# Kernel optimization log

Measured on AMD Instinct MI355X. Metric: run time of the kernel, lower is better.

Reference implementation:

```python
import jax, jax.numpy as jnp
import numpy as np

N_HEAD, D_MODEL, D_HEAD = 16, 1024, 64
SEQ, BATCH = 1024, 8
SCALE = 1.0 / (D_HEAD ** 0.5)
LN_EPS = 1e-5


def setup_inputs() -> dict:
    key = jax.random.key(0)
    ks = jax.random.split(key, 16)
    dk = N_HEAD * D_HEAD  # == D_MODEL
    init_qkv = 1.0 / np.sqrt(D_MODEL)
    init_out = 1.0 / np.sqrt(dk)
    u = lambda k, shp, lo, hi: jax.random.uniform(k, shp, jnp.float32, lo, hi)
    inp = {
        'dec_inp': jax.random.normal(ks[0], (SEQ, BATCH, D_MODEL), jnp.float32),
        'attn_mask': jnp.triu(jnp.ones((SEQ, SEQ), dtype=bool), k=1),  # causal
        'query_mean': u(ks[1], (dk, D_MODEL), -init_qkv, init_qkv),
        'key_mean': u(ks[2], (dk, D_MODEL), -init_qkv, init_qkv),
        'value_mean': u(ks[3], (dk, D_MODEL), -init_qkv, init_qkv),
        'query_std': u(ks[4], (dk, D_MODEL), 2 * np.log(init_qkv), np.log(init_qkv)),
        'key_std': u(ks[5], (dk, D_MODEL), 2 * np.log(init_qkv), np.log(init_qkv)),
        'value_std': u(ks[6], (dk, D_MODEL), 2 * np.log(init_qkv), np.log(init_qkv)),
        'output_mean': u(ks[7], (D_MODEL, dk), -init_out, init_out),
        'output_std': u(ks[8], (D_MODEL, dk), 2 * np.log(init_out), np.log(init_out)),
        'ln_gamma': jnp.ones((D_MODEL,), jnp.float32),
        'ln_beta': jnp.zeros((D_MODEL,), jnp.float32),
        # per-forward reparameterization noise (training mode)
        'eps_q': jax.random.normal(ks[9], (dk, D_MODEL), jnp.float32),
        'eps_k': jax.random.normal(ks[10], (dk, D_MODEL), jnp.float32),
        'eps_v': jax.random.normal(ks[11], (dk, D_MODEL), jnp.float32),
        'eps_o': jax.random.normal(ks[12], (D_MODEL, dk), jnp.float32),
    }
    return inp


def _forward(dec_inp, query_mean, key_mean, value_mean, query_std, key_std,
             value_std, output_mean, output_std, ln_gamma, ln_beta,
             eps_q, eps_k, eps_v, eps_o, attn_mask):
    S, B, _ = dec_inp.shape
    # Bayesian weight sampling: w = mean + eps * exp(std)
    qw = query_mean + eps_q * jnp.exp(query_std)
    kw = key_mean + eps_k * jnp.exp(key_std)
    vw = value_mean + eps_v * jnp.exp(value_std)
    # NOTE: original code (bug kept for faithfulness) builds the output weight
    # from value_mean + output_diff, not output_mean.
    ow = value_mean + eps_o * jnp.exp(output_std)

    head_q = (dec_inp @ qw.T).reshape(S, B, N_HEAD, D_HEAD)
    head_k = (dec_inp @ kw.T).reshape(S, B, N_HEAD, D_HEAD)
    head_v = (dec_inp @ vw.T).reshape(S, B, N_HEAD, D_HEAD)

    score = jnp.einsum('ibnd,jbnd->ijbn', head_q, head_k) * SCALE
    score = jnp.where(attn_mask[:, :, None, None], -jnp.inf, score)
    prob = jax.nn.softmax(score, axis=1)  # softmax over j (key) axis
    attn_vec = jnp.einsum('ijbn,jbnd->ibnd', prob, head_v).reshape(S, B, N_HEAD * D_HEAD)

    attn_out = attn_vec @ ow.T
    x = dec_inp + attn_out
    mu = jnp.mean(x, axis=-1, keepdims=True)
    var = jnp.var(x, axis=-1, keepdims=True)
    output = (x - mu) * jax.lax.rsqrt(var + LN_EPS) * ln_gamma + ln_beta

    theta_mean = jnp.concatenate([query_mean, key_mean, value_mean, output_mean.T], -1)
    theta_std = jnp.concatenate([query_std, key_std, value_std, output_std.T], -1)
    kl = jnp.mean(theta_mean ** 2 - theta_std * 2.0 + jnp.exp(theta_std * 2.0)) / 2.0
    return output, kl


def reference(dec_inp, attn_mask, query_mean, key_mean, value_mean, query_std,
              key_std, value_std, output_mean, output_std, ln_gamma, ln_beta,
              eps_q, eps_k, eps_v, eps_o):
    return _forward(dec_inp, query_mean, key_mean, value_mean, query_std,
                    key_std, value_std, output_mean, output_std, ln_gamma,
                    ln_beta, eps_q, eps_k, eps_v, eps_o, attn_mask)
```

## Files before the change

kernel.cpp:

```cpp
#include <hip/hip_runtime.h>

typedef _Float16 f16x8 __attribute__((ext_vector_type(8)));
typedef _Float16 f16x4 __attribute__((ext_vector_type(4)));
typedef float    f32x4 __attribute__((ext_vector_type(4)));

static __device__ __forceinline__ f32x4 mfma16(f16x8 a, f16x8 b, f32x4 c) {
    return __builtin_amdgcn_mfma_f32_16x16x32_f16(a, b, c, 0, 0, 0);
}

static __device__ __forceinline__ void gload_lds16(const _Float16* g, _Float16* lds) {
    __builtin_amdgcn_global_load_lds(
        (const __attribute__((address_space(1))) unsigned int*)g,
        (__attribute__((address_space(3))) unsigned int*)lds, 16, 0, 0);
}

__global__ __launch_bounds__(256) void k_prep(
    const float* __restrict__ qm, const float* __restrict__ km, const float* __restrict__ vm,
    const float* __restrict__ qs, const float* __restrict__ ks, const float* __restrict__ vs,
    const float* __restrict__ om, const float* __restrict__ os,
    const float* __restrict__ eq, const float* __restrict__ ek,
    const float* __restrict__ ev, const float* __restrict__ eo,
    _Float16* __restrict__ wq, _Float16* __restrict__ wk,
    _Float16* __restrict__ wv, _Float16* __restrict__ wo,
    float* __restrict__ part,
    const float* __restrict__ dec, _Float16* __restrict__ xh)
{
    if (blockIdx.x >= 1024) {
        int base = (blockIdx.x - 1024) * 4096;
        #pragma unroll
        for (int rp = 0; rp < 4; ++rp) {
            int i = base + rp * 1024 + threadIdx.x * 4;
            float4 v = *(const float4*)&dec[i];
            f16x4 hv;
            hv[0] = (_Float16)v.x; hv[1] = (_Float16)v.y;
            hv[2] = (_Float16)v.z; hv[3] = (_Float16)v.w;
            *(f16x4*)&xh[i] = hv;
        }
        return;
    }
    int i = (blockIdx.x * 256 + threadIdx.x) * 4;
    f32x4 aqm = *(const f32x4*)&qm[i], akm = *(const f32x4*)&km[i], avm = *(const f32x4*)&vm[i];
    f32x4 aqs = *(const f32x4*)&qs[i], aks = *(const f32x4*)&ks[i], avs = *(const f32x4*)&vs[i];
    f32x4 aom = *(const f32x4*)&om[i], aos = *(const f32x4*)&os[i];
    f32x4 veq = *(const f32x4*)&eq[i], vek = *(const f32x4*)&ek[i];
    f32x4 vev = *(const f32x4*)&ev[i], veo = *(const f32x4*)&eo[i];
    f16x4 hq, hk, hv, ho;
    float t = 0.f;
    #pragma unroll
    for (int j = 0; j < 4; ++j) {
        hq[j] = (_Float16)(aqm[j] + veq[j] * __expf(aqs[j]));
        hk[j] = (_Float16)(akm[j] + vek[j] * __expf(aks[j]));
        hv[j] = (_Float16)(avm[j] + vev[j] * __expf(avs[j]));
        ho[j] = (_Float16)(avm[j] + veo[j] * __expf(aos[j]));
        t += aqm[j]*aqm[j] - 2.f*aqs[j] + __expf(2.f*aqs[j])
           + akm[j]*akm[j] - 2.f*aks[j] + __expf(2.f*aks[j])
           + avm[j]*avm[j] - 2.f*avs[j] + __expf(2.f*avs[j])
           + aom[j]*aom[j] - 2.f*aos[j] + __expf(2.f*aos[j]);
    }
    *(f16x4*)&wq[i] = hq;
    *(f16x4*)&wk[i] = hk;
    *(f16x4*)&wv[i] = hv;
    *(f16x4*)&wo[i] = ho;
    #pragma unroll
    for (int m = 1; m < 64; m <<= 1) t += __shfl_xor(t, m, 64);
    __shared__ float red[4];
    int w = threadIdx.x >> 6, lane = threadIdx.x & 63;
    if (lane == 0) red[w] = t;
    __syncthreads();
    if (threadIdx.x == 0) part[blockIdx.x] = red[0] + red[1] + red[2] + red[3];
}

__global__ __launch_bounds__(256) void k_gemm(
    const _Float16* __restrict__ A, const _Float16* __restrict__ Bp,
    _Float16* __restrict__ Cp, const float* __restrict__ resid,
    float* __restrict__ xout, int mode, float sc)
{
    __shared__ __align__(16) _Float16 As[128 * 64];
    __shared__ __align__(16) _Float16 Bs[128 * 64];
    const int K = 1024, N = 1024;
    int flat = blockIdx.y * 8 + blockIdx.x;
    int xcd = flat & 7, j = flat >> 3;
    int tM = (xcd * 8 + (j & 7)) * 128;
    int tN = (j >> 3) * 128;
    int tid = threadIdx.x, w = tid >> 6, lane = tid & 63;
    int wm = w & 1, wn = w >> 1;
    int q = lane >> 4, r = lane & 15;
    int csrc = ((lane & 7) ^ (lane >> 3)) * 8;
    int srow = lane >> 3;
    f32x4 acc[4][4] = {};
    for (int kk = 0; kk < K; kk += 64) {
        __syncthreads();
        #pragma unroll
        for (int i = 0; i < 4; ++i) {
            int chunk = w * 4 + i;
            int row = chunk * 8 + srow;
            gload_lds16(A  + (size_t)(tM + row) * K + kk + csrc, &As[chunk * 512]);
            gload_lds16(Bp + (size_t)(tN + row) * K + kk + csrc, &Bs[chunk * 512]);
        }
        __syncthreads();
        #pragma unroll
        for (int kc = 0; kc < 2; ++kc) {
            f16x8 af[4], bf[4];
            #pragma unroll
            for (int m = 0; m < 4; ++m) {
                int row = wm*64 + m*16 + r;
                int pos = ((kc*4 + q) ^ (r & 7)) * 8;
                af[m] = *(const f16x8*)&As[row*64 + pos];
            }
            #pragma unroll
            for (int n = 0; n < 4; ++n) {
                int row = wn*64 + n*16 + r;
                int pos = ((kc*4 + q) ^ (r & 7)) * 8;
                bf[n] = *(const f16x8*)&Bs[row*64 + pos];
            }
            #pragma unroll
            for (int m = 0; m < 4; ++m)
                #pragma unroll
                for (int n = 0; n < 4; ++n)
                    acc[m][n] = mfma16(af[m], bf[n], acc[m][n]);
        }
    }
    #pragma unroll
    for (int m = 0; m < 4; ++m)
      #pragma unroll
      for (int n = 0; n < 4; ++n)
        #pragma unroll
        for (int t = 0; t < 4; ++t) {
            int row = tM + wm*64 + m*16 + q*4 + t;
            int col = tN + wn*64 + n*16 + r;
            size_t o = (size_t)row * N + col;
            if (mode == 0) Cp[o] = (_Float16)(acc[m][n][t] * sc);
            else           xout[o] = resid[o] + acc[m][n][t];
        }
}

__global__ __launch_bounds__(256) void k_vtrans(const _Float16* __restrict__ V,
                                                _Float16* __restrict__ Vt)
{
    __shared__ __align__(16) _Float16 L[64 * 72];
    int c = blockIdx.x;
    int b = c >> 4, h = c & 15;
    int s0 = blockIdx.y * 64;
    int tid = threadIdx.x;
    #pragma unroll
    for (int rep = 0; rep < 2; ++rep) {
        int idx = rep * 256 + tid;
        int sl = idx >> 3, ch = idx & 7;
        f16x8 v = *(const f16x8*)&V[((size_t)(s0 + sl) * 8 + b) * 1024 + h * 64 + ch * 8];
        *(f16x8*)&L[sl * 72 + ch * 8] = v;
    }
    __syncthreads();
    #pragma unroll
    for (int rep = 0; rep < 2; ++rep) {
        int idx = rep * 256 + tid;
        int d = idx >> 3, c2 = idx & 7;
        f16x8 o;
        #pragma unroll
        for (int e = 0; e < 8; ++e) o[e] = L[(c2 * 8 + e) * 72 + d];
        *(f16x8*)&Vt[((size_t)c * 64 + d) * 1024 + s0 + c2 * 8] = o;
    }
}

__global__ __launch_bounds__(256, 3) void k_attn(
    const _Float16* __restrict__ Qb, const _Float16* __restrict__ Kb,
    const _Float16* __restrict__ Vtg, _Float16* __restrict__ AVo)
{
    __shared__ __align__(16) _Float16 Ks[2][64 * 64];
    __shared__ __align__(16) _Float16 Vs[2][64 * 64];
    __shared__ __align__(16) _Float16 Ps[4 * 32 * 72];
    const int bh = blockIdx.x;
    const int b = bh & 7, h = bh >> 3;
    const int cbh = b * 16 + h;
    const int qt = (0x15623740u >> (blockIdx.y * 4)) & 7;
    const int tid = threadIdx.x, w = tid >> 6, lane = tid & 63;
    const int q = lane >> 4, r = lane & 15;
    const int i0 = qt * 128 + w * 32;
    const int csrc = ((lane & 7) ^ (lane >> 3)) * 8;
    const int srow = lane >> 3;

    f16x8 qf[2][2];
    #pragma unroll
    for (int it = 0; it < 2; ++it)
      #pragma unroll
      for (int kc = 0; kc < 2; ++kc)
        qf[it][kc] = *(const f16x8*)&Qb[((size_t)(i0 + it*16 + r)*8 + b)*1024 + h*64 + kc*32 + q*8];

    f32x4 ot[4][2] = {};
    float mrun[2] = {-1e30f, -1e30f}, lrun[2] = {0.f, 0.f};
    _Float16* Pw = &Ps[w * 2304];

    auto stage = [&](int kt, int buf) __attribute__((always_inline)) {
        #pragma unroll
        for (int ii = 0; ii < 2; ++ii) {
            int chunk = w * 2 + ii;
            int row = chunk * 8 + srow;
            gload_lds16(Kb  + ((size_t)(kt*64 + row)*8 + b)*1024 + h*64 + csrc, &Ks[buf][chunk*512]);
            gload_lds16(Vtg + ((size_t)(cbh*64 + row))*1024 + kt*64 + csrc,     &Vs[buf][chunk*512]);
        }
    };

    auto tile = [&](int kt, int buf, bool MASK) __attribute__((always_inline)) {
        f32x4 st[4][2] = {};
        #pragma unroll
        for (int kc = 0; kc < 2; ++kc) {
            f16x8 kf[4];
            #pragma unroll
            for (int jt = 0; jt < 4; ++jt) {
                int pos = ((kc*4 + q) ^ (r & 7)) * 8;
                kf[jt] = *(const f16x8*)&Ks[buf][(jt*16 + r)*64 + pos];
            }
            __builtin_amdgcn_s_setprio(1);
            #pragma unroll
            for (int jt = 0; jt < 4; ++jt)
              #pragma unroll
              for (int it = 0; it < 2; ++it)
                st[jt][it] = mfma16(kf[jt], qf[it][kc], st[jt][it]);
            __builtin_amdgcn_s_setprio(0);
        }

        #pragma unroll
        for (int it = 0; it < 2; ++it) {
            if (MASK) {
                int il = i0 + it*16 + r;
                #pragma unroll
                for (int jt = 0; jt < 4; ++jt)
                  #pragma unroll
                  for (int t = 0; t < 4; ++t)
                    if (kt*64 + jt*16 + q*4 + t > il) st[jt][it][t] = -1e30f;
            }
            float mx = -1e30f;
            #pragma unroll
            for (int jt = 0; jt < 4; ++jt) {
                f32x4 s4 = st[jt][it];
                mx = fmaxf(mx, fmaxf(fmaxf(s4[0], s4[1]), fmaxf(s4[2], s4[3])));
            }
            mx = fmaxf(mx, __shfl_xor(mx, 16, 64));
            mx = fmaxf(mx, __shfl_xor(mx, 32, 64));
            if (!__all(mx - mrun[it] <= 8.f)) {
                float mnew = fmaxf(mrun[it], mx);
                float al = __expf(mrun[it] - mnew);
                lrun[it] *= al;
                #pragma unroll
                for (int dtb = 0; dtb < 4; ++dtb) ot[dtb][it] *= al;
                mrun[it] = mnew;
            }
            float mref = mrun[it];
            float ps = 0.f;
            #pragma unroll
            for (int jt = 0; jt < 4; ++jt) {
                f16x4 hv;
                #pragma unroll
                for (int t = 0; t < 4; ++t) {
                    float e = __expf(st[jt][it][t] - mref);
                    ps += e;
                    hv[t] = (_Float16)e;
                }
                *(f16x4*)&Pw[(it*16 + r)*72 + jt*16 + q*4] = hv;
            }
            ps += __shfl_xor(ps, 16, 64);
            ps += __shfl_xor(ps, 32, 64);
            lrun[it] += ps;
        }

        #pragma unroll
        for (int kc = 0; kc < 2; ++kc) {
            f16x8 vf[4], pf[2];
            #pragma unroll
            for (int dtb = 0; dtb < 4; ++dtb) {
                int pos = ((kc*4 + q) ^ (r & 7)) * 8;
                vf[dtb] = *(const f16x8*)&Vs[buf][(dtb*16 + r)*64 + pos];
            }
            #pragma unroll
            for (int it = 0; it < 2; ++it)
                pf[it] = *(const f16x8*)&Pw[(it*16 + r)*72 + kc*32 + q*8];
            __builtin_amdgcn_s_setprio(1);
            #pragma unroll
            for (int dtb = 0; dtb < 4; ++dtb)
              #pragma unroll
              for (int it = 0; it < 2; ++it)
                ot[dtb][it] = mfma16(vf[dtb], pf[it], ot[dtb][it]);
            __builtin_amdgcn_s_setprio(0);
        }
    };

    stage(0, 0);
    __syncthreads();
    for (int kt = 0; kt < 2*qt; ++kt) {
        stage(kt + 1, (kt + 1) & 1);
        tile(kt, kt & 1, false);
        __syncthreads();
    }
    {
        int kt = 2*qt;
        stage(kt + 1, (kt + 1) & 1);
        tile(kt, kt & 1, true);
        __syncthreads();
        tile(kt + 1, (kt + 1) & 1, true);
    }

    #pragma unroll
    for (int it = 0; it < 2; ++it) {
        float inv = 1.f / lrun[it];
        int s = i0 + it*16 + r;
        #pragma unroll
        for (int dtb = 0; dtb < 4; ++dtb) {
            f16x4 hv;
            #pragma unroll
            for (int t = 0; t < 4; ++t) hv[t] = (_Float16)(ot[dtb][it][t] * inv);
            *(f16x4*)&AVo[((size_t)s*8 + b)*1024 + h*64 + dtb*16 + q*4] = hv;
        }
    }
}

__global__ __launch_bounds__(256) void k_ln(float* __restrict__ x,
    const float* __restrict__ g, const float* __restrict__ bta,
    const float* __restrict__ part)
{
    int w = threadIdx.x >> 6, lane = threadIdx.x & 63;
    if (blockIdx.x == 2048) {
        __shared__ float rs[4];
        float s = 0.f;
        for (int i = threadIdx.x; i < 1024; i += 256) s += part[i];
        #pragma unroll
        for (int m = 1; m < 64; m <<= 1) s += __shfl_xor(s, m, 64);
        if (lane == 0) rs[w] = s;
        __syncthreads();
        if (threadIdx.x == 0)
            x[8388608] = (rs[0] + rs[1] + rs[2] + rs[3]) * (0.5f / 4194304.f);
        return;
    }
    int row = blockIdx.x * 4 + w;
    float* xr = x + (size_t)row * 1024;
    float4 v[4];
    float s = 0.f, s2 = 0.f;
    #pragma unroll
    for (int rp = 0; rp < 4; ++rp) {
        v[rp] = *(const float4*)&xr[rp * 256 + lane * 4];
        s  += v[rp].x + v[rp].y + v[rp].z + v[rp].w;
        s2 += v[rp].x*v[rp].x + v[rp].y*v[rp].y + v[rp].z*v[rp].z + v[rp].w*v[rp].w;
    }
    #pragma unroll
    for (int m = 1; m < 64; m <<= 1) { s += __shfl_xor(s, m, 64); s2 += __shfl_xor(s2, m, 64); }
    float mu = s * (1.f / 1024.f);
    float var = s2 * (1.f / 1024.f) - mu * mu;
    float rstd = rsqrtf(var + 1e-5f);
    #pragma unroll
    for (int rp = 0; rp < 4; ++rp) {
        float4 gv = *(const float4*)&g[rp * 256 + lane * 4];
        float4 bv = *(const float4*)&bta[rp * 256 + lane * 4];
        float4 ov;
        ov.x = (v[rp].x - mu) * rstd * gv.x + bv.x;
        ov.y = (v[rp].y - mu) * rstd * gv.y + bv.y;
        ov.z = (v[rp].z - mu) * rstd * gv.z + bv.z;
        ov.w = (v[rp].w - mu) * rstd * gv.w + bv.w;
        *(float4*)&xr[rp * 256 + lane * 4] = ov;
    }
}

extern "C" void kernel_launch(void* const* d_in, const int* in_sizes, int n_in,
                              void* d_out, int out_size, void* d_ws, size_t ws_size,
                              hipStream_t stream)
{
    (void)in_sizes; (void)n_in; (void)out_size; (void)ws_size;
    const float* dec   = (const float*)d_in[0];
    const float* qm    = (const float*)d_in[2];
    const float* km    = (const float*)d_in[3];
    const float* vm    = (const float*)d_in[4];
    const float* qs    = (const float*)d_in[5];
    const float* ks    = (const float*)d_in[6];
    const float* vs    = (const float*)d_in[7];
    const float* om    = (const float*)d_in[8];
    const float* os    = (const float*)d_in[9];
    const float* gamma = (const float*)d_in[10];
    const float* beta  = (const float*)d_in[11];
    const float* eq    = (const float*)d_in[12];
    const float* ek    = (const float*)d_in[13];
    const float* ev    = (const float*)d_in[14];
    const float* eo    = (const float*)d_in[15];

    char* ws = (char*)d_ws;
    _Float16* WQ   = (_Float16*)ws;
    float*    PART = (float*)(ws + (8ull  << 20));
    _Float16* XH   = (_Float16*)(ws + (9ull  << 20));
    _Float16* Qh   = (_Float16*)(ws + (25ull << 20));
    _Float16* Kh   = Qh + 8388608;
    _Float16* Vh   = Qh + 16777216;
    _Float16* Vtg  = XH;
    _Float16* AV   = Vh;
    float*    out  = (float*)d_out;

    k_prep<<<dim3(3072), dim3(256), 0, stream>>>(
        qm, km, vm, qs, ks, vs, om, os, eq, ek, ev, eo,
        WQ, WQ + 1048576, WQ + 2097152, WQ + 3145728, PART, dec, XH);
    k_gemm<<<dim3(8, 64), dim3(256), 0, stream>>>(XH, WQ,           Qh, dec, out, 0, 0.125f);
    k_gemm<<<dim3(8, 64), dim3(256), 0, stream>>>(XH, WQ + 1048576, Kh, dec, out, 0, 1.0f);
    k_gemm<<<dim3(8, 64), dim3(256), 0, stream>>>(XH, WQ + 2097152, Vh, dec, out, 0, 1.0f);
    k_vtrans<<<dim3(128, 16), dim3(256), 0, stream>>>(Vh, Vtg);
    k_attn<<<dim3(128, 8), dim3(256), 0, stream>>>(Qh, Kh, Vtg, AV);
    k_gemm<<<dim3(8, 64), dim3(256), 0, stream>>>(AV, WQ + 3145728, Qh, dec, out, 1, 1.0f);
    k_ln<<<dim3(2049), dim3(256), 0, stream>>>(out, gamma, beta, PART);
}
```

Baseline: 312.5 us.

## Keep softmax probabilities in registers via bpermute and batch QKV GEMMs

In the attention kernel the P tile no longer goes through LDS. Probabilities are packed to fp16 pairs and reshuffled across lanes with ds_bpermute into the MFMA B-operand layout, which frees the LDS buffer and raises launch bounds from 3 to 4 waves-groups per CU. The three Q/K/V projection GEMMs are merged into one launch using blockIdx.z, with the Q scale chosen per z-slice. Round-toward-zero conversion slightly changes the rounding of P, and the extra bpermutes and selects add instruction and register pressure.

New measurement: 323.6 us. +3.6%, slower.

```diff
diff --git a/kernel.cpp b/kernel.cpp
--- a/kernel.cpp
+++ b/kernel.cpp
@@ -12,6 +12,12 @@
     __builtin_amdgcn_global_load_lds(
         (const __attribute__((address_space(1))) unsigned int*)g,
         (__attribute__((address_space(3))) unsigned int*)lds, 16, 0, 0);
+}
+
+static __device__ __forceinline__ int pkrtz(float a, float b) {
+    union { decltype(__builtin_amdgcn_cvt_pkrtz(0.f, 0.f)) h; int u; } c;
+    c.h = __builtin_amdgcn_cvt_pkrtz(a, b);
+    return c.u;
 }
 
 __global__ __launch_bounds__(256) void k_prep(
@@ -71,13 +77,15 @@
 }
 
 __global__ __launch_bounds__(256) void k_gemm(
-    const _Float16* __restrict__ A, const _Float16* __restrict__ Bp,
-    _Float16* __restrict__ Cp, const float* __restrict__ resid,
-    float* __restrict__ xout, int mode, float sc)
+    const _Float16* __restrict__ A, const _Float16* __restrict__ B0,
+    _Float16* __restrict__ C0, const float* __restrict__ resid,
+    float* __restrict__ xout, int mode)
 {
     __shared__ __align__(16) _Float16 As[128 * 64];
     __shared__ __align__(16) _Float16 Bs[128 * 64];
     const int K = 1024, N = 1024;
+    const _Float16* Bp = B0 + (size_t)blockIdx.z * 1048576u;
+    _Float16* Cp = C0 + (size_t)blockIdx.z * 8388608u;
     int flat = blockIdx.y * 8 + blockIdx.x;
     int xcd = flat & 7, j = flat >> 3;
     int tM = (xcd * 8 + (j & 7)) * 128;
@@ -120,6 +128,7 @@
                     acc[m][n] = mfma16(af[m], bf[n], acc[m][n]);
         }
     }
+    float sc = (mode == 0 && blockIdx.z == 0) ? 0.125f : 1.0f;
     #pragma unroll
     for (int m = 0; m < 4; ++m)
       #pragma unroll
@@ -161,13 +170,12 @@
     }
 }
 
-__global__ __launch_bounds__(256, 3) void k_attn(
+__global__ __launch_bounds__(256, 4) void k_attn(
     const _Float16* __restrict__ Qb, const _Float16* __restrict__ Kb,
     const _Float16* __restrict__ Vtg, _Float16* __restrict__ AVo)
 {
     __shared__ __align__(16) _Float16 Ks[2][64 * 64];
     __shared__ __align__(16) _Float16 Vs[2][64 * 64];
-    __shared__ __align__(16) _Float16 Ps[4 * 32 * 72];
     const int bh = blockIdx.x;
     const int b = bh & 7, h = bh >> 3;
     const int cbh = b * 16 + h;
@@ -177,6 +185,9 @@
     const int i0 = qt * 128 + w * 32;
     const int csrc = ((lane & 7) ^ (lane >> 3)) * 8;
     const int srow = lane >> 3;
+    const int idx0 = (((q & 1) * 2) * 16 + r) * 4;
+    const int idx1 = idx0 + 64;
+    const bool hisel = (lane & 32) != 0;
 
     f16x8 qf[2][2];
     #pragma unroll
@@ -187,7 +198,6 @@
 
     f32x4 ot[4][2] = {};
     float mrun[2] = {-1e30f, -1e30f}, lrun[2] = {0.f, 0.f};
-    _Float16* Pw = &Ps[w * 2304];
 
     auto stage = [&](int kt, int buf) __attribute__((always_inline)) {
         #pragma unroll
@@ -218,6 +228,7 @@
             __builtin_amdgcn_s_setprio(0);
         }
 
+        f16x8 pfr[2][2];
         #pragma unroll
         for (int it = 0; it < 2; ++it) {
             if (MASK) {
@@ -246,39 +257,57 @@
             }
             float mref = mrun[it];
             float ps = 0.f;
+            int pk[4][2];
             #pragma unroll
             for (int jt = 0; jt < 4; ++jt) {
-                f16x4 hv;
-                #pragma unroll
-                for (int t = 0; t < 4; ++t) {
-                    float e = __expf(st[jt][it][t] - mref);
-                    ps += e;
-                    hv[t] = (_Float16)e;
-                }
-                *(f16x4*)&Pw[(it*16 + r)*72 + jt*16 + q*4] = hv;
+                float p0 = __expf(st[jt][it][0] - mref);
+                float p1 = __expf(st[jt][it][1] - mref);
+                float p2 = __expf(st[jt][it][2] - mref);
+                float p3 = __expf(st[jt][it][3] - mref);
+                ps += (p0 + p1) + (p2 + p3);
+                pk[jt][0] = pkrtz(p0, p1);
+                pk[jt][1] = pkrtz(p2, p3);
             }
             ps += __shfl_xor(ps, 16, 64);
             ps += __shfl_xor(ps, 32, 64);
             lrun[it] += ps;
+            int b0[4][2], b1[4][2];
+            #pragma unroll
+            for (int jt = 0; jt < 4; ++jt)
+              #pragma unroll
+              for (int p = 0; p < 2; ++p) {
+                  b0[jt][p] = __builtin_amdgcn_ds_bpermute(idx0, pk[jt][p]);
+                  b1[jt][p] = __builtin_amdgcn_ds_bpermute(idx1, pk[jt][p]);
+              }
+            #pragma unroll
+            for (int kc = 0; kc < 2; ++kc) {
+                union { int u[4]; f16x8 v; } pu;
+                #pragma unroll
+                for (int s = 0; s < 2; ++s)
+                  #pragma unroll
+                  for (int p = 0; p < 2; ++p) {
+                      int lo = s ? b1[2*kc][p]     : b0[2*kc][p];
+                      int hi = s ? b1[2*kc + 1][p] : b0[2*kc + 1][p];
+                      pu.u[2*s + p] = hisel ? hi : lo;
+                  }
+                pfr[it][kc] = pu.v;
+            }
         }
 
         #pragma unroll
         for (int kc = 0; kc < 2; ++kc) {
-            f16x8 vf[4], pf[2];
+            f16x8 vf[4];
             #pragma unroll
             for (int dtb = 0; dtb < 4; ++dtb) {
                 int pos = ((kc*4 + q) ^ (r & 7)) * 8;
                 vf[dtb] = *(const f16x8*)&Vs[buf][(dtb*16 + r)*64 + pos];
             }
-            #pragma unroll
-            for (int it = 0; it < 2; ++it)
-                pf[it] = *(const f16x8*)&Pw[(it*16 + r)*72 + kc*32 + q*8];
             __builtin_amdgcn_s_setprio(1);
             #pragma unroll
             for (int dtb = 0; dtb < 4; ++dtb)
               #pragma unroll
               for (int it = 0; it < 2; ++it)
-                ot[dtb][it] = mfma16(vf[dtb], pf[it], ot[dtb][it]);
+                ot[dtb][it] = mfma16(vf[dtb], pfr[it][kc], ot[dtb][it]);
             __builtin_amdgcn_s_setprio(0);
         }
     };
@@ -392,11 +421,9 @@
     k_prep<<<dim3(3072), dim3(256), 0, stream>>>(
         qm, km, vm, qs, ks, vs, om, os, eq, ek, ev, eo,
         WQ, WQ + 1048576, WQ + 2097152, WQ + 3145728, PART, dec, XH);
-    k_gemm<<<dim3(8, 64), dim3(256), 0, stream>>>(XH, WQ,           Qh, dec, out, 0, 0.125f);
-    k_gemm<<<dim3(8, 64), dim3(256), 0, stream>>>(XH, WQ + 1048576, Kh, dec, out, 0, 1.0f);
-    k_gemm<<<dim3(8, 64), dim3(256), 0, stream>>>(XH, WQ + 2097152, Vh, dec, out, 0, 1.0f);
+    k_gemm<<<dim3(8, 64, 3), dim3(256), 0, stream>>>(XH, WQ, Qh, dec, out, 0);
     k_vtrans<<<dim3(128, 16), dim3(256), 0, stream>>>(Vh, Vtg);
     k_attn<<<dim3(128, 8), dim3(256), 0, stream>>>(Qh, Kh, Vtg, AV);
-    k_gemm<<<dim3(8, 64), dim3(256), 0, stream>>>(AV, WQ + 3145728, Qh, dec, out, 1, 1.0f);
+    k_gemm<<<dim3(8, 64, 1), dim3(256), 0, stream>>>(AV, WQ + 3145728, Qh, dec, out, 1);
     k_ln<<<dim3(2049), dim3(256), 0, stream>>>(out, gamma, beta, PART);
 }
```
